# Performance work log

Measured on AMD Instinct MI355X. Metric: run time of the kernel, lower is better.

Reference implementation:

```python
import jax, jax.numpy as jnp
import numpy as np
from math import pi as PI

N = 50000      # nodes
E = 800000     # edges
G = 512        # graphs
L = 6          # num_layers
D = 128        # hidden_channels
F = 128        # num_filters
NG = 50        # num_gaussians
IN = 28        # input_dim
OUT = 32       # out_channels
CUT = 6.0      # cutoff
LN2 = float(np.log(2.0))
BN_EPS = 1e-5


def ssp(x):
    # ShiftedSoftplus
    return jax.nn.softplus(x) - LN2


def setup_inputs() -> dict:
    key = jax.random.key(0)
    ks = jax.random.split(key, 16)
    def rn(i, shape, s=0.05):
        return jax.random.normal(ks[i], shape, dtype=jnp.float32) * s
    return {
        "x": jax.random.normal(ks[0], (N, IN), dtype=jnp.float32),
        "pos": jax.random.normal(ks[1], (N, 3), dtype=jnp.float32) * 3.0,
        "batch": jnp.sort(jax.random.randint(ks[2], (N,), 0, G)),
        "edge_index": jax.random.randint(ks[3], (2, E), 0, N),
        # FeatureEmbedding: Linear(28,64) -> BN(64) -> ReLU -> Linear(64,128) -> ReLU
        "fe_w1": rn(4, (IN, D // 2)), "fe_b1": jnp.zeros((D // 2,), jnp.float32),
        "bn_gamma": jnp.ones((D // 2,), jnp.float32), "bn_beta": jnp.zeros((D // 2,), jnp.float32),
        "fe_w2": rn(5, (D // 2, D)), "fe_b2": jnp.zeros((D,), jnp.float32),
        # per-layer update_e: lin (no bias), mlp: Linear(NG,F)->SSP->Linear(F,F)
        "lin_w": rn(6, (L, D, F)),
        "mlp_w1": rn(7, (L, NG, F)), "mlp_b1": jnp.zeros((L, F), jnp.float32),
        "mlp_w2": rn(8, (L, F, F)), "mlp_b2": jnp.zeros((L, F), jnp.float32),
        # per-layer update_v: Linear(F,D)->SSP->Linear(D,D), residual
        "v1_w": rn(9, (L, F, D)), "v1_b": jnp.zeros((L, D), jnp.float32),
        "v2_w": rn(10, (L, D, D)), "v2_b": jnp.zeros((L, D), jnp.float32),
        # update_u: Linear(D,D//2)->SSP->Linear(D//2,OUT), then scatter over graphs
        "u1_w": rn(11, (D, D // 2)), "u1_b": jnp.zeros((D // 2,), jnp.float32),
        "u2_w": rn(12, (D // 2, OUT)), "u2_b": jnp.zeros((OUT,), jnp.float32),
    }


def reference(x, pos, batch, edge_index,
              fe_w1, fe_b1, bn_gamma, bn_beta, fe_w2, fe_b2,
              lin_w, mlp_w1, mlp_b1, mlp_w2, mlp_b2,
              v1_w, v1_b, v2_w, v2_b,
              u1_w, u1_b, u2_w, u2_b):
    row, col = edge_index[0], edge_index[1]  # (j, i): gather source j, scatter target i
    d = pos[row] - pos[col]                  # [E,3]
    dist = jnp.sqrt(jnp.sum(d * d, axis=-1))  # [E]
    offset = jnp.linspace(0.0, CUT, NG)
    coeff = -0.5 / (offset[1] - offset[0]) ** 2
    dist_emb = jnp.exp(coeff * (dist[:, None] - offset[None, :]) ** 2)  # [E,NG]
    cosC = 0.5 * (jnp.cos(dist * PI / CUT) + 1.0)                        # [E]

    # FeatureEmbedding (BatchNorm in training mode: batch statistics)
    h = x @ fe_w1 + fe_b1
    mu = jnp.mean(h, axis=0)
    var = jnp.mean((h - mu) ** 2, axis=0)
    h = (h - mu) / jnp.sqrt(var + BN_EPS) * bn_gamma + bn_beta
    h = jax.nn.relu(h)
    v = jax.nn.relu(h @ fe_w2 + fe_b2)  # [N,D]

    for l in range(L):
        # update_e: gate MLP on gaussian embedding, cosine cutoff, gather v[j]
        W = (ssp(dist_emb @ mlp_w1[l] + mlp_b1[l]) @ mlp_w2[l] + mlp_b2[l]) * cosC[:, None]  # [E,F]
        e = (v @ lin_w[l])[row] * W                                                          # [E,F]
        # update_v: scatter-add to nodes, MLP, residual
        agg = jax.ops.segment_sum(e, col, num_segments=N)                                    # [N,F]
        v = v + (ssp(agg @ v1_w[l] + v1_b[l]) @ v2_w[l] + v2_b[l])

    # update_u: per-node MLP then scatter-add per graph
    s = ssp(v @ u1_w + u1_b) @ u2_w + u2_b  # [N,OUT]
    return jax.ops.segment_sum(s, batch, num_segments=G)  # [G,OUT]
```

## Files before the change

### kernel.cpp

```cpp
#include <hip/hip_runtime.h>
#include <hip/hip_fp16.h>
#include <math.h>

#define DEV __device__ __forceinline__

constexpr int NGAUSS = 50;
constexpr int LAY = 6;
constexpr int K_TAB = 8192;
constexpr float DMAX = 40.0f;
constexpr float TSCALE = (float)(K_TAB - 1) / DMAX;
constexpr float STEP = 6.0f / 49.0f;
constexpr float COEFF = -0.5f / (STEP * STEP);
constexpr float LN2F = 0.69314718055994531f;
constexpr float PI_OVER_CUT = 0.52359877559829887f;

using f16x8 = __attribute__((ext_vector_type(8))) _Float16;
using f16x4 = __attribute__((ext_vector_type(4))) _Float16;
using f32x4 = __attribute__((ext_vector_type(4))) float;
using f32x8 = __attribute__((ext_vector_type(8))) float;

#define MFMA16(a, b, c) __builtin_amdgcn_mfma_f32_16x16x32_f16(a, b, c, 0, 0, 0)

DEV float sspf(float x) {
    float ax = fabsf(x);
    float e = __expf(-ax);
    return fmaxf(x, 0.f) + __logf(1.f + e) - LN2F;
}

DEV float4 ld_h4(const ushort* p) {
    uint2 r = *(const uint2*)p;
    __half2 a = __builtin_bit_cast(__half2, r.x);
    __half2 b = __builtin_bit_cast(__half2, r.y);
    float2 fa = __half22float2(a), fb = __half22float2(b);
    return make_float4(fa.x, fa.y, fb.x, fb.y);
}

__global__ void k_cvtT128(const float* __restrict__ src, ushort* __restrict__ dst) {
    const float* s = src + (size_t)blockIdx.x * 16384;
    ushort* d = dst + (size_t)blockIdx.x * 16384;
    for (int i = threadIdx.x; i < 16384; i += 256) {
        int k = i >> 7, c = i & 127;
        d[(c << 7) + k] = __builtin_bit_cast(ushort, (_Float16)s[i]);
    }
}
__global__ void k_cvtT_fe(const float* __restrict__ src, ushort* __restrict__ dst) {
    for (int i = threadIdx.x; i < 8192; i += 256) {
        int k = i >> 7, c = i & 127;
        dst[(c << 6) + k] = __builtin_bit_cast(ushort, (_Float16)src[i]);
    }
}
__global__ void k_cvtT_w1(const float* __restrict__ src, ushort* __restrict__ dst) {
    const float* s = src + (size_t)blockIdx.x * (NGAUSS * 128);
    ushort* d = dst + (size_t)blockIdx.x * (128 * 64);
    for (int i = threadIdx.x; i < 128 * 64; i += 256) {
        int c = i >> 6, k = i & 63;
        float v = (k < NGAUSS) ? s[k * 128 + c] : 0.f;
        d[(c << 6) + k] = __builtin_bit_cast(ushort, (_Float16)v);
    }
}

__global__ void k_hist(const int* __restrict__ ei, int* __restrict__ counts, int E) {
    int e = blockIdx.x * 256 + threadIdx.x;
    if (e < E) atomicAdd(&counts[ei[E + e]], 1);
}

__global__ void k_scan1(const int* __restrict__ counts, int* __restrict__ locex,
                        int* __restrict__ bsum, int n) {
    __shared__ int s_wsum[16];
    const int tid = threadIdx.x;
    const int i = blockIdx.x * 1024 + tid;
    const int lane = tid & 63, wv = tid >> 6;
    int v = (i < n) ? counts[i] : 0;
    int x = v;
    #pragma unroll
    for (int off = 1; off < 64; off <<= 1) {
        int y = __shfl_up(x, off, 64);
        if (lane >= off) x += y;
    }
    if (lane == 63) s_wsum[wv] = x;
    __syncthreads();
    if (wv == 0 && lane < 16) {
        int wval = s_wsum[lane];
        int wx = wval;
        #pragma unroll
        for (int off = 1; off < 16; off <<= 1) {
            int wy = __shfl_up(wx, off, 16);
            if (lane >= off) wx += wy;
        }
        s_wsum[lane] = wx - wval;
    }
    __syncthreads();
    if (i < n) locex[i] = s_wsum[wv] + x - v;
    if (tid == 1023) bsum[blockIdx.x] = s_wsum[15] + x;
}

__global__ void k_scan2(int* __restrict__ bsum, int nb) {
    __shared__ int s_wsum[16];
    const int tid = threadIdx.x;
    const int lane = tid & 63, wv = tid >> 6;
    int v = (tid < nb) ? bsum[tid] : 0;
    int x = v;
    #pragma unroll
    for (int off = 1; off < 64; off <<= 1) {
        int y = __shfl_up(x, off, 64);
        if (lane >= off) x += y;
    }
    if (lane == 63) s_wsum[wv] = x;
    __syncthreads();
    if (wv == 0 && lane < 16) {
        int wval = s_wsum[lane];
        int wx = wval;
        #pragma unroll
        for (int off = 1; off < 16; off <<= 1) {
            int wy = __shfl_up(wx, off, 16);
            if (lane >= off) wx += wy;
        }
        s_wsum[lane] = wx - wval;
    }
    __syncthreads();
    if (tid < nb) bsum[tid] = s_wsum[wv] + x - v;
}

__global__ void k_scan3(const int* __restrict__ locex, const int* __restrict__ bsumex,
                        int* __restrict__ cursor, int* __restrict__ rowptr, int n) {
    int i = blockIdx.x * 256 + threadIdx.x;
    if (i >= n) return;
    int e = locex[i] + bsumex[i >> 10];
    cursor[i] = e;
    rowptr[i] = e;
}

__global__ void k_scatter(const int* __restrict__ ei, const float* __restrict__ pos,
                          int* __restrict__ cursor, uint* __restrict__ s_ef, int E) {
    int e = blockIdx.x * 256 + threadIdx.x;
    if (e >= E) return;
    int r = ei[e], c = ei[E + e];
    int p = atomicAdd(&cursor[c], 1);
    float dx = pos[3 * r + 0] - pos[3 * c + 0];
    float dy = pos[3 * r + 1] - pos[3 * c + 1];
    float dz = pos[3 * r + 2] - pos[3 * c + 2];
    float d = sqrtf(dx * dx + dy * dy + dz * dz);
    int i0 = (int)(d * TSCALE + 0.5f);
    if (i0 > K_TAB - 1) i0 = K_TAB - 1;
    s_ef[p] = (uint)r | ((uint)i0 << 16);
}

__launch_bounds__(256)
__global__ void k_tab_all(const ushort* __restrict__ w1TA, const float* __restrict__ b1A,
                          const ushort* __restrict__ w2TA, const float* __restrict__ b2A,
                          ushort* __restrict__ tabA) {
    const int layer = blockIdx.x / (K_TAB / 32);
    const int k0 = (blockIdx.x % (K_TAB / 32)) * 32;
    const ushort* w1T = w1TA + (size_t)layer * 8192;
    const float* b1 = b1A + (size_t)layer * 128;
    const ushort* w2T = w2TA + (size_t)layer * 16384;
    const float* b2 = b2A + (size_t)layer * 128;
    ushort* tab = tabA + (size_t)layer * K_TAB * 128;

    constexpr int LDD = 72;
    constexpr int LDP = 136;
    __shared__ _Float16 sD[32 * LDD];
    __shared__ _Float16 sT[32 * LDP];
    __shared__ float s_cc[32];
    const int tid = threadIdx.x;

    for (int i = tid; i < 32 * 64; i += 256) {
        int r = i >> 6, g = i & 63;
        float val = 0.f;
        if (g < NGAUSS) {
            float d = (float)(k0 + r) * (1.0f / TSCALE);
            float t = d - g * STEP;
            val = __expf(COEFF * t * t);
        }
        sD[r * LDD + g] = (_Float16)val;
    }
    if (tid < 32) {
        float d = (float)(k0 + tid) * (1.0f / TSCALE);
        s_cc[tid] = 0.5f * (__cosf(d * PI_OVER_CUT) + 1.0f);
    }
    __syncthreads();

    const int wid = tid >> 6, lane = tid & 63;
    const int lr = lane & 15, lg = lane >> 4;
    const int kof = lg << 3;

    #pragma unroll
    for (int cb = 0; cb < 2; cb++) {
        const int col = ((2 * wid + cb) << 4) + lr;
        const ushort* bp = w1T + ((size_t)col << 6);
        f16x8 B0 = *(const f16x8*)(bp + kof);
        f16x8 B1 = *(const f16x8*)(bp + 32 + kof);
        float bb = b1[col];
        #pragma unroll
        for (int rt = 0; rt < 2; rt++) {
            const _Float16* ap = &sD[((rt << 4) + lr) * LDD + kof];
            f32x4 c = {0.f, 0.f, 0.f, 0.f};
            c = MFMA16(*(const f16x8*)ap, B0, c);
            c = MFMA16(*(const f16x8*)(ap + 32), B1, c);
            #pragma unroll
            for (int r = 0; r < 4; r++)
                sT[((rt << 4) + (lg << 2) + r) * LDP + col] = (_Float16)sspf(c[r] + bb);
        }
    }
    __syncthreads();

    #pragma unroll
    for (int cb = 0; cb < 2; cb++) {
        const int col = ((2 * wid + cb) << 4) + lr;
        const ushort* bp = w2T + ((size_t)col << 7);
        f16x8 B0 = *(const f16x8*)(bp + kof);
        f16x8 B1 = *(const f16x8*)(bp + 32 + kof);
        f16x8 B2 = *(const f16x8*)(bp + 64 + kof);
        f16x8 B3 = *(const f16x8*)(bp + 96 + kof);
        float bb = b2[col];
        #pragma unroll
        for (int rt = 0; rt < 2; rt++) {
            const _Float16* ap = &sT[((rt << 4) + lr) * LDP + kof];
            f32x4 c = {0.f, 0.f, 0.f, 0.f};
            c = MFMA16(*(const f16x8*)ap, B0, c);
            c = MFMA16(*(const f16x8*)(ap + 32), B1, c);
            c = MFMA16(*(const f16x8*)(ap + 64), B2, c);
            c = MFMA16(*(const f16x8*)(ap + 96), B3, c);
            #pragma unroll
            for (int r = 0; r < 4; r++) {
                int kr = (rt << 4) + (lg << 2) + r;
                tab[((size_t)(k0 + kr) << 7) + col] =
                    __builtin_bit_cast(ushort, (_Float16)((c[r] + bb) * s_cc[kr]));
            }
        }
    }
}

__launch_bounds__(256, 8)
__global__ void k_edge_csr(const uint* __restrict__ s_ef,
                           const int* __restrict__ rowptr, const int* __restrict__ counts,
                           const ushort* __restrict__ vlin, const ushort* __restrict__ tab,
                           ushort* __restrict__ agg, int N) {
    const int tid = threadIdx.x;
    const int l32 = tid & 31;
    const int h = l32 >> 4;
    const int lc = l32 & 15;
    const int n = blockIdx.x * 8 + (tid >> 5);
    if (n >= N) return;
    const ushort* tabc = tab + (lc << 3);
    const ushort* vlc  = vlin + (lc << 3);

    const int rs = rowptr[n];
    const int re = rs + counts[n];
    f32x8 acc = {0.f, 0.f, 0.f, 0.f, 0.f, 0.f, 0.f, 0.f};

    int e = rs + h;
    for (; e + 6 < re; e += 8) {
        f16x8 TP[4], VL[4];
        #pragma unroll
        for (int j = 0; j < 4; j++) {
            uint pk = s_ef[e + 2 * j];
            TP[j] = *(const f16x8*)(tabc + ((size_t)(pk >> 16) << 7));
            VL[j] = *(const f16x8*)(vlc + ((size_t)(pk & 0xFFFFu) << 7));
        }
        f16x8 p0 = TP[0] * VL[0];
        p0 += TP[1] * VL[1];
        f16x8 p1 = TP[2] * VL[2];
        p1 += TP[3] * VL[3];
        acc += __builtin_convertvector(p0, f32x8);
        acc += __builtin_convertvector(p1, f32x8);
    }
    for (; e < re; e += 2) {
        uint pk = s_ef[e];
        f16x8 tp = *(const f16x8*)(tabc + ((size_t)(pk >> 16) << 7));
        f16x8 vl = *(const f16x8*)(vlc + ((size_t)(pk & 0xFFFFu) << 7));
        acc += __builtin_convertvector(tp * vl, f32x8);
    }
    #pragma unroll
    for (int i = 0; i < 8; i++) acc[i] += __shfl_xor(acc[i], 16);
    if (h == 0) {
        f16x8 o;
        #pragma unroll
        for (int i = 0; i < 8; i++) o[i] = (_Float16)acc[i];
        *(f16x8*)&agg[((size_t)n << 7) + (lc << 3)] = o;
    }
}

__global__ void k_fe1(const float* __restrict__ x, const float* __restrict__ w,
                      const float* __restrict__ b, float* __restrict__ h, int N) {
    int idx = blockIdx.x * 256 + threadIdx.x;
    if (idx >= N * 64) return;
    int n = idx >> 6, c = idx & 63;
    const float* xr = x + (size_t)n * 28;
    float acc = b[c];
    #pragma unroll
    for (int k = 0; k < 28; k++) acc = fmaf(xr[k], w[k * 64 + c], acc);
    h[idx] = acc;
}

__global__ void k_bnstat(const float* __restrict__ h, float* __restrict__ stats, int N) {
    __shared__ float s_s[256], s_q[256];
    int tid = threadIdx.x;
    int c = tid & 63, g = tid >> 6;
    float s = 0.f, q = 0.f;
    for (int n = blockIdx.x * 4 + g; n < N; n += gridDim.x * 4) {
        float v = h[(size_t)n * 64 + c];
        s += v; q += v * v;
    }
    s_s[tid] = s; s_q[tid] = q;
    __syncthreads();
    if (tid < 64) {
        s = s_s[tid] + s_s[tid + 64] + s_s[tid + 128] + s_s[tid + 192];
        q = s_q[tid] + s_q[tid + 64] + s_q[tid + 128] + s_q[tid + 192];
        atomicAdd(&stats[tid], s);
        atomicAdd(&stats[64 + tid], q);
    }
}

__global__ void k_bnfin(const float* __restrict__ stats, float* __restrict__ prm,
                        const float* __restrict__ gamma, const float* __restrict__ beta,
                        float invN) {
    int c = threadIdx.x;
    float mu = stats[c] * invN;
    float var = stats[64 + c] * invN - mu * mu;
    float sc = gamma[c] * rsqrtf(var + 1e-5f);
    prm[c] = sc;
    prm[64 + c] = beta[c] - mu * sc;
}

__launch_bounds__(256, 4)
__global__ void k_fe2(const float* __restrict__ h, const float* __restrict__ prm,
                      const ushort* __restrict__ w2T, const float* __restrict__ b2,
                      ushort* __restrict__ v16, int N) {
    constexpr int LDP = 72;
    __shared__ _Float16 sH[64 * LDP];
    const int tid = threadIdx.x;
    const int n0 = blockIdx.x * 64;

    for (int i = tid; i < 64 * 16; i += 256) {
        int row = i >> 4, c4 = (i & 15) << 2;
        int gr = n0 + row;
        float4 hv = (gr < N) ? *(const float4*)&h[((size_t)gr << 6) + c4]
                             : make_float4(0.f, 0.f, 0.f, 0.f);
        float4 sc = *(const float4*)&prm[c4];
        float4 sh = *(const float4*)&prm[64 + c4];
        f16x4 o;
        o[0] = (_Float16)fmaxf(fmaf(hv.x, sc.x, sh.x), 0.f);
        o[1] = (_Float16)fmaxf(fmaf(hv.y, sc.y, sh.y), 0.f);
        o[2] = (_Float16)fmaxf(fmaf(hv.z, sc.z, sh.z), 0.f);
        o[3] = (_Float16)fmaxf(fmaf(hv.w, sc.w, sh.w), 0.f);
        *(f16x4*)&sH[row * LDP + c4] = o;
    }
    __syncthreads();

    const int wid = tid >> 6, lane = tid & 63;
    const int lr = lane & 15, lg = lane >> 4;
    const int kof = lg << 3;
    const int arow = wid * 16 + lr;
    const int drow0 = wid * 16 + (lg << 2);

    f16x8 a0 = *(const f16x8*)&sH[arow * LDP + kof];
    f16x8 a1 = *(const f16x8*)&sH[arow * LDP + 32 + kof];

    #pragma unroll
    for (int n = 0; n < 8; n++) {
        const ushort* bp = w2T + (((size_t)(n << 4) + lr) << 6);
        f32x4 c = {0.f, 0.f, 0.f, 0.f};
        c = MFMA16(a0, *(const f16x8*)(bp + kof), c);
        c = MFMA16(a1, *(const f16x8*)(bp + 32 + kof), c);
        int col = (n << 4) + lr;
        float bb = b2[col];
        #pragma unroll
        for (int r = 0; r < 4; r++) {
            int gr = n0 + drow0 + r;
            if (gr < N) v16[((size_t)gr << 7) + col] =
                __builtin_bit_cast(ushort, (_Float16)fmaxf(c[r] + bb, 0.f));
        }
    }
}

__launch_bounds__(256, 4)
__global__ void k_gemm_rb(const ushort* __restrict__ A, const ushort* __restrict__ wT,
                          ushort* __restrict__ C, int N) {
    constexpr int LDP = 136;
    __shared__ _Float16 sA[64 * LDP];
    const int tid = threadIdx.x;
    const int n0 = blockIdx.x * 64;

    for (int i = tid; i < 64 * 32; i += 256) {
        int row = i >> 5, c4 = (i & 31) << 2;
        int gr = n0 + row;
        uint2 val = (gr < N) ? *(const uint2*)&A[((size_t)gr << 7) + c4]
                             : make_uint2(0u, 0u);
        *(uint2*)&sA[row * LDP + c4] = val;
    }
    __syncthreads();

    const int wid = tid >> 6, lane = tid & 63;
    const int lr = lane & 15, lg = lane >> 4;
    const int kof = lg << 3;
    const int arow = wid * 16 + lr;
    const int drow0 = wid * 16 + (lg << 2);

    f16x8 a0 = *(const f16x8*)&sA[arow * LDP + kof];
    f16x8 a1 = *(const f16x8*)&sA[arow * LDP + 32 + kof];
    f16x8 a2 = *(const f16x8*)&sA[arow * LDP + 64 + kof];
    f16x8 a3 = *(const f16x8*)&sA[arow * LDP + 96 + kof];

    #pragma unroll
    for (int n = 0; n < 8; n++) {
        const ushort* bp = wT + (((size_t)(n << 4) + lr) << 7);
        f32x4 c = {0.f, 0.f, 0.f, 0.f};
        c = MFMA16(a0, *(const f16x8*)(bp + kof), c);
        c = MFMA16(a1, *(const f16x8*)(bp + 32 + kof), c);
        c = MFMA16(a2, *(const f16x8*)(bp + 64 + kof), c);
        c = MFMA16(a3, *(const f16x8*)(bp + 96 + kof), c);
        int col = (n << 4) + lr;
        #pragma unroll
        for (int r = 0; r < 4; r++) {
            int gr = n0 + drow0 + r;
            if (gr < N) C[((size_t)gr << 7) + col] =
                __builtin_bit_cast(ushort, (_Float16)c[r]);
        }
    }
}

__launch_bounds__(512, 8)
__global__ void k_update(const ushort* __restrict__ agg,
                         const ushort* __restrict__ w1T, const float* __restrict__ b1,
                         const ushort* __restrict__ w2T, const float* __restrict__ b2,
                         ushort* __restrict__ v16,
                         const ushort* __restrict__ linT, ushort* __restrict__ vlin, int N) {
    constexpr int LDP = 136;
    __shared__ _Float16 sA[64 * LDP];
    __shared__ _Float16 sB[64 * LDP];
    const int tid = threadIdx.x;
    const int n0 = blockIdx.x * 64;

    for (int i = tid; i < 64 * 32; i += 512) {
        int row = i >> 5, c4 = (i & 31) << 2;
        int gr = n0 + row;
        uint2 a = (gr < N) ? *(const uint2*)&agg[((size_t)gr << 7) + c4] : make_uint2(0u, 0u);
        uint2 b = (gr < N) ? *(const uint2*)&v16[((size_t)gr << 7) + c4] : make_uint2(0u, 0u);
        *(uint2*)&sA[row * LDP + c4] = a;
        *(uint2*)&sB[row * LDP + c4] = b;
    }
    __syncthreads();

    const int wid = tid >> 6, lane = tid & 63;
    const int lr = lane & 15, lg = lane >> 4;
    const int kof = lg << 3;
    const int col = (wid << 4) + lr;
    const int dr0 = lg << 2;

    f32x4 acc[4];

    {
        const ushort* bp = w1T + ((size_t)col << 7);
        f16x8 B0 = *(const f16x8*)(bp + kof);
        f16x8 B1 = *(const f16x8*)(bp + 32 + kof);
        f16x8 B2 = *(const f16x8*)(bp + 64 + kof);
        f16x8 B3 = *(const f16x8*)(bp + 96 + kof);
        #pragma unroll
        for (int rb = 0; rb < 4; rb++) {
            const _Float16* ap = &sA[((rb << 4) + lr) * LDP + kof];
            f32x4 c = {0.f, 0.f, 0.f, 0.f};
            c = MFMA16(*(const f16x8*)ap, B0, c);
            c = MFMA16(*(const f16x8*)(ap + 32), B1, c);
            c = MFMA16(*(const f16x8*)(ap + 64), B2, c);
            c = MFMA16(*(const f16x8*)(ap + 96), B3, c);
            acc[rb] = c;
        }
    }
    __syncthreads();
    {
        float bb = b1[col];
        #pragma unroll
        for (int rb = 0; rb < 4; rb++) {
            #pragma unroll
            for (int r = 0; r < 4; r++)
                sA[((rb << 4) + dr0 + r) * LDP + col] = (_Float16)sspf(acc[rb][r] + bb);
        }
    }
    __syncthreads();

    {
        const ushort* bp = w2T + ((size_t)col << 7);
        f16x8 B0 = *(const f16x8*)(bp + kof);
        f16x8 B1 = *(const f16x8*)(bp + 32 + kof);
        f16x8 B2 = *(const f16x8*)(bp + 64 + kof);
        f16x8 B3 = *(const f16x8*)(bp + 96 + kof);
        #pragma unroll
        for (int rb = 0; rb < 4; rb++) {
            const _Float16* ap = &sA[((rb << 4) + lr) * LDP + kof];
            f32x4 c = {0.f, 0.f, 0.f, 0.f};
            c = MFMA16(*(const f16x8*)ap, B0, c);
            c = MFMA16(*(const f16x8*)(ap + 32), B1, c);
            c = MFMA16(*(const f16x8*)(ap + 64), B2, c);
            c = MFMA16(*(const f16x8*)(ap + 96), B3, c);
            acc[rb] = c;
        }
    }
    {
        float bb = b2[col];
        #pragma unroll
        for (int rb = 0; rb < 4; rb++) {
            #pragma unroll
            for (int r = 0; r < 4; r++) {
                _Float16* p = &sB[((rb << 4) + dr0 + r) * LDP + col];
                *p = (_Float16)(acc[rb][r] + bb + (float)*p);
            }
        }
    }
    __syncthreads();

    for (int i = tid; i < 64 * 32; i += 512) {
        int row = i >> 5, c4 = (i & 31) << 2;
        int gr = n0 + row;
        if (gr < N) *(uint2*)&v16[((size_t)gr << 7) + c4] = *(const uint2*)&sB[row * LDP + c4];
    }
    if (!linT) return;

    {
        const ushort* bp = linT + ((size_t)col << 7);
        f16x8 B0 = *(const f16x8*)(bp + kof);
        f16x8 B1 = *(const f16x8*)(bp + 32 + kof);
        f16x8 B2 = *(const f16x8*)(bp + 64 + kof);
        f16x8 B3 = *(const f16x8*)(bp + 96 + kof);
        #pragma unroll
        for (int rb = 0; rb < 4; rb++) {
            const _Float16* ap = &sB[((rb << 4) + lr) * LDP + kof];
            f32x4 c = {0.f, 0.f, 0.f, 0.f};
            c = MFMA16(*(const f16x8*)ap, B0, c);
            c = MFMA16(*(const f16x8*)(ap + 32), B1, c);
            c = MFMA16(*(const f16x8*)(ap + 64), B2, c);
            c = MFMA16(*(const f16x8*)(ap + 96), B3, c);
            acc[rb] = c;
        }
    }
    #pragma unroll
    for (int rb = 0; rb < 4; rb++) {
        #pragma unroll
        for (int r = 0; r < 4; r++)
            sA[((rb << 4) + dr0 + r) * LDP + col] = (_Float16)acc[rb][r];
    }
    __syncthreads();

    for (int i = tid; i < 64 * 32; i += 512) {
        int row = i >> 5, c4 = (i & 31) << 2;
        int gr = n0 + row;
        if (gr < N) *(uint2*)&vlin[((size_t)gr << 7) + c4] = *(const uint2*)&sA[row * LDP + c4];
    }
}

__launch_bounds__(256, 4)
__global__ void k_uout(const ushort* __restrict__ v16, const float* __restrict__ u1w,
                       const float* __restrict__ u1b, const float* __restrict__ u2w,
                       const float* __restrict__ u2b, const int* __restrict__ batch,
                       float* __restrict__ out, int N) {
    __shared__ float sA[64 * 128];
    const int tid = threadIdx.x;
    const int n0 = blockIdx.x * 64;

    for (int i = tid; i < 64 * 32; i += 256) {
        int row = i >> 5, cq = (i & 31) << 2;
        int gr = n0 + row;
        float4 val = make_float4(0.f, 0.f, 0.f, 0.f);
        if (gr < N) val = ld_h4(&v16[((size_t)gr << 7) + cq]);
        *(float4*)&sA[row * 128 + cq] = val;
    }
    __syncthreads();

    const int cg = tid & 31, rg = tid >> 5;
    const int r0 = rg << 3;
    const int c2 = cg << 1;

    float2 acc[8];
    {
        float2 b1v = *(const float2*)&u1b[c2];
        #pragma unroll
        for (int i = 0; i < 8; i++) acc[i] = b1v;
        #pragma unroll 4
        for (int k = 0; k < 128; k++) {
            float2 wv = *(const float2*)&u1w[(k << 6) + c2];
            #pragma unroll
            for (int i = 0; i < 8; i++) {
                float a = sA[(r0 + i) * 128 + k];
                acc[i].x = fmaf(a, wv.x, acc[i].x);
                acc[i].y = fmaf(a, wv.y, acc[i].y);
            }
        }
    }
    __syncthreads();
    #pragma unroll
    for (int i = 0; i < 8; i++) {
        sA[(r0 + i) * 64 + c2 + 0] = sspf(acc[i].x);
        sA[(r0 + i) * 64 + c2 + 1] = sspf(acc[i].y);
    }
    __syncthreads();

    float acc2[8];
    {
        float bb = u2b[cg];
        #pragma unroll
        for (int i = 0; i < 8; i++) acc2[i] = bb;
        #pragma unroll 4
        for (int k = 0; k < 64; k++) {
            float wv = u2w[(k << 5) + cg];
            #pragma unroll
            for (int i = 0; i < 8; i++)
                acc2[i] = fmaf(sA[(r0 + i) * 64 + k], wv, acc2[i]);
        }
    }

    int cur = -1;
    float run = 0.f;
    #pragma unroll
    for (int i = 0; i < 8; i++) {
        int gr = n0 + r0 + i;
        int g = (gr < N) ? batch[gr] : -1;
        if (g != cur) {
            if (cur >= 0) atomicAdd(&out[(size_t)cur * 32 + cg], run);
            cur = g;
            run = 0.f;
        }
        if (g >= 0) run += acc2[i];
    }
    if (cur >= 0) atomicAdd(&out[(size_t)cur * 32 + cg], run);
}

extern "C" void kernel_launch(void* const* d_in, const int* in_sizes, int n_in,
                              void* d_out, int out_size, void* d_ws, size_t ws_size,
                              hipStream_t stream) {
    const float* x      = (const float*)d_in[0];
    const float* pos    = (const float*)d_in[1];
    const int*   batch  = (const int*)d_in[2];
    const int*   ei     = (const int*)d_in[3];
    const float* fe_w1  = (const float*)d_in[4];
    const float* fe_b1  = (const float*)d_in[5];
    const float* bn_g   = (const float*)d_in[6];
    const float* bn_b   = (const float*)d_in[7];
    const float* fe_w2  = (const float*)d_in[8];
    const float* fe_b2  = (const float*)d_in[9];
    const float* lin_w  = (const float*)d_in[10];
    const float* mlp_w1 = (const float*)d_in[11];
    const float* mlp_b1 = (const float*)d_in[12];
    const float* mlp_w2 = (const float*)d_in[13];
    const float* mlp_b2 = (const float*)d_in[14];
    const float* v1_w   = (const float*)d_in[15];
    const float* v1_b   = (const float*)d_in[16];
    const float* v2_w   = (const float*)d_in[17];
    const float* v2_b   = (const float*)d_in[18];
    const float* u1_w   = (const float*)d_in[19];
    const float* u1_b   = (const float*)d_in[20];
    const float* u2_w   = (const float*)d_in[21];
    const float* u2_b   = (const float*)d_in[22];

    const int N = in_sizes[0] / 28;
    const int E = in_sizes[3] / 2;
    const int NB1 = (N + 1023) / 1024;

    char* ws = (char*)d_ws;
    size_t o = 0;
    auto alloc = [&](size_t bytes) { void* p = ws + o; o += (bytes + 255) & ~(size_t)255; return p; };
    int*    counts = (int*)   alloc((size_t)N * 4);
    int*    cursor = (int*)   alloc((size_t)N * 4);
    int*    rowptr = (int*)   alloc((size_t)N * 4);
    int*    bsum   = (int*)   alloc((size_t)NB1 * 4);
    uint*   s_ef   = (uint*)  alloc((size_t)E * 4);
    float*  stats  = (float*) alloc(128 * 4);
    float*  prm    = (float*) alloc(128 * 4);
    ushort* tab    = (ushort*)alloc((size_t)LAY * K_TAB * 128 * 2);
    ushort* v16    = (ushort*)alloc((size_t)N * 128 * 2);
    ushort* vlin   = (ushort*)alloc((size_t)N * 128 * 2);
    ushort* agg    = (ushort*)alloc((size_t)N * 128 * 2);
    float*  h      = (float*) alloc((size_t)N * 64 * 4);
    int*    locex  = (int*)   alloc((size_t)N * 4);
    ushort* v1T    = (ushort*)alloc((size_t)LAY * 16384 * 2);
    ushort* v2T    = (ushort*)alloc((size_t)LAY * 16384 * 2);
    ushort* linT   = (ushort*)alloc((size_t)LAY * 16384 * 2);
    ushort* mw2T   = (ushort*)alloc((size_t)LAY * 16384 * 2);
    ushort* mw1T   = (ushort*)alloc((size_t)LAY * 8192 * 2);
    ushort* fe2T   = (ushort*)alloc((size_t)8192 * 2);

    k_cvtT128<<<LAY, 256, 0, stream>>>(v1_w, v1T);
    k_cvtT128<<<LAY, 256, 0, stream>>>(v2_w, v2T);
    k_cvtT128<<<LAY, 256, 0, stream>>>(lin_w, linT);
    k_cvtT128<<<LAY, 256, 0, stream>>>(mlp_w2, mw2T);
    k_cvtT_w1<<<LAY, 256, 0, stream>>>(mlp_w1, mw1T);
    k_cvtT_fe<<<1, 256, 0, stream>>>(fe_w2, fe2T);

    hipMemsetAsync(counts, 0, (size_t)N * 4, stream);
    k_hist<<<(E + 255) / 256, 256, 0, stream>>>(ei, counts, E);
    k_scan1<<<NB1, 1024, 0, stream>>>(counts, locex, bsum, N);
    k_scan2<<<1, 1024, 0, stream>>>(bsum, NB1);
    k_scan3<<<(N + 255) / 256, 256, 0, stream>>>(locex, bsum, cursor, rowptr, N);
    k_scatter<<<(E + 255) / 256, 256, 0, stream>>>(ei, pos, cursor, s_ef, E);

    k_tab_all<<<LAY * (K_TAB / 32), 256, 0, stream>>>(mw1T, mlp_b1, mw2T, mlp_b2, tab);

    hipMemsetAsync(stats, 0, 128 * 4, stream);
    k_fe1<<<(N * 64 + 255) / 256, 256, 0, stream>>>(x, fe_w1, fe_b1, h, N);
    k_bnstat<<<256, 256, 0, stream>>>(h, stats, N);
    k_bnfin<<<1, 64, 0, stream>>>(stats, prm, bn_g, bn_b, 1.0f / (float)N);
    const int gblk = (N + 63) / 64;
    k_fe2<<<gblk, 256, 0, stream>>>(h, prm, fe2T, fe_b2, v16, N);

    k_gemm_rb<<<gblk, 256, 0, stream>>>(v16, linT, vlin, N);

    const int eblk = (N + 7) / 8;
    for (int l = 0; l < LAY; l++) {
        k_edge_csr<<<eblk, 256, 0, stream>>>(
            s_ef, rowptr, counts, vlin,
            tab + (size_t)l * K_TAB * 128, agg, N);
        const ushort* lin_next = (l + 1 < LAY) ? linT + (size_t)(l + 1) * 16384 : nullptr;
        k_update<<<gblk, 512, 0, stream>>>(
            agg, v1T + (size_t)l * 16384, v1_b + (size_t)l * 128,
            v2T + (size_t)l * 16384, v2_b + (size_t)l * 128,
            v16, lin_next, vlin, N);
    }

    hipMemsetAsync(d_out, 0, (size_t)out_size * 4, stream);
    k_uout<<<gblk, 256, 0, stream>>>(v16, u1_w, u1_b, u2_w, u2_b, batch, (float*)d_out, N);
}
```

Before: 601.4 us.

## Record atomic rank in histogram and widen edge aggregation to one wavefront per node

The histogram kernel now stores each edge's atomic rank, so the scatter computes its CSR slot as rowptr plus rank and no longer needs a second atomic pass or a cursor array. The per-node edge aggregation kernel now assigns a full 64-lane wavefront (four edge streams) to each node instead of half a wavefront (two streams), with an extra cross-lane shuffle reduction. This aims to cut contended atomics in setup and raise memory-level parallelism in the gather loop. The cost is an extra E-sized rank buffer and more idle lanes on nodes with few edges.

```diff
diff --git a/kernel.cpp b/kernel.cpp
--- a/kernel.cpp
+++ b/kernel.cpp
@@ -59,9 +59,10 @@
     }
 }
 
-__global__ void k_hist(const int* __restrict__ ei, int* __restrict__ counts, int E) {
+__global__ void k_hist(const int* __restrict__ ei, int* __restrict__ counts,
+                       int* __restrict__ rank, int E) {
     int e = blockIdx.x * 256 + threadIdx.x;
-    if (e < E) atomicAdd(&counts[ei[E + e]], 1);
+    if (e < E) rank[e] = atomicAdd(&counts[ei[E + e]], 1);
 }
 
 __global__ void k_scan1(const int* __restrict__ counts, int* __restrict__ locex,
@@ -122,26 +123,25 @@
 }
 
 __global__ void k_scan3(const int* __restrict__ locex, const int* __restrict__ bsumex,
-                        int* __restrict__ cursor, int* __restrict__ rowptr, int n) {
+                        int* __restrict__ rowptr, int n) {
     int i = blockIdx.x * 256 + threadIdx.x;
     if (i >= n) return;
-    int e = locex[i] + bsumex[i >> 10];
-    cursor[i] = e;
-    rowptr[i] = e;
+    rowptr[i] = locex[i] + bsumex[i >> 10];
 }
 
 __global__ void k_scatter(const int* __restrict__ ei, const float* __restrict__ pos,
-                          int* __restrict__ cursor, uint* __restrict__ s_ef, int E) {
+                          const int* __restrict__ rowptr, const int* __restrict__ rank,
+                          uint* __restrict__ s_ef, int E) {
     int e = blockIdx.x * 256 + threadIdx.x;
     if (e >= E) return;
     int r = ei[e], c = ei[E + e];
-    int p = atomicAdd(&cursor[c], 1);
     float dx = pos[3 * r + 0] - pos[3 * c + 0];
     float dy = pos[3 * r + 1] - pos[3 * c + 1];
     float dz = pos[3 * r + 2] - pos[3 * c + 2];
     float d = sqrtf(dx * dx + dy * dy + dz * dz);
     int i0 = (int)(d * TSCALE + 0.5f);
     if (i0 > K_TAB - 1) i0 = K_TAB - 1;
+    int p = rowptr[c] + rank[e];
     s_ef[p] = (uint)r | ((uint)i0 << 16);
 }
 
@@ -237,10 +237,10 @@
                            const ushort* __restrict__ vlin, const ushort* __restrict__ tab,
                            ushort* __restrict__ agg, int N) {
     const int tid = threadIdx.x;
-    const int l32 = tid & 31;
-    const int h = l32 >> 4;
-    const int lc = l32 & 15;
-    const int n = blockIdx.x * 8 + (tid >> 5);
+    const int lane = tid & 63;
+    const int h = lane >> 4;
+    const int lc = lane & 15;
+    const int n = blockIdx.x * 4 + (tid >> 6);
     if (n >= N) return;
     const ushort* tabc = tab + (lc << 3);
     const ushort* vlc  = vlin + (lc << 3);
@@ -250,11 +250,11 @@
     f32x8 acc = {0.f, 0.f, 0.f, 0.f, 0.f, 0.f, 0.f, 0.f};
 
     int e = rs + h;
-    for (; e + 6 < re; e += 8) {
+    for (; e + 12 < re; e += 16) {
         f16x8 TP[4], VL[4];
         #pragma unroll
         for (int j = 0; j < 4; j++) {
-            uint pk = s_ef[e + 2 * j];
+            uint pk = s_ef[e + 4 * j];
             TP[j] = *(const f16x8*)(tabc + ((size_t)(pk >> 16) << 7));
             VL[j] = *(const f16x8*)(vlc + ((size_t)(pk & 0xFFFFu) << 7));
         }
@@ -265,14 +265,17 @@
         acc += __builtin_convertvector(p0, f32x8);
         acc += __builtin_convertvector(p1, f32x8);
     }
-    for (; e < re; e += 2) {
+    for (; e < re; e += 4) {
         uint pk = s_ef[e];
         f16x8 tp = *(const f16x8*)(tabc + ((size_t)(pk >> 16) << 7));
         f16x8 vl = *(const f16x8*)(vlc + ((size_t)(pk & 0xFFFFu) << 7));
         acc += __builtin_convertvector(tp * vl, f32x8);
     }
     #pragma unroll
-    for (int i = 0; i < 8; i++) acc[i] += __shfl_xor(acc[i], 16);
+    for (int i = 0; i < 8; i++) {
+        acc[i] += __shfl_xor(acc[i], 16);
+        acc[i] += __shfl_xor(acc[i], 32);
+    }
     if (h == 0) {
         f16x8 o;
         #pragma unroll
@@ -659,9 +662,9 @@
     size_t o = 0;
     auto alloc = [&](size_t bytes) { void* p = ws + o; o += (bytes + 255) & ~(size_t)255; return p; };
     int*    counts = (int*)   alloc((size_t)N * 4);
-    int*    cursor = (int*)   alloc((size_t)N * 4);
     int*    rowptr = (int*)   alloc((size_t)N * 4);
     int*    bsum   = (int*)   alloc((size_t)NB1 * 4);
+    int*    rank   = (int*)   alloc((size_t)E * 4);
     uint*   s_ef   = (uint*)  alloc((size_t)E * 4);
     float*  stats  = (float*) alloc(128 * 4);
     float*  prm    = (float*) alloc(128 * 4);
@@ -686,11 +689,11 @@
     k_cvtT_fe<<<1, 256, 0, stream>>>(fe_w2, fe2T);
 
     hipMemsetAsync(counts, 0, (size_t)N * 4, stream);
-    k_hist<<<(E + 255) / 256, 256, 0, stream>>>(ei, counts, E);
+    k_hist<<<(E + 255) / 256, 256, 0, stream>>>(ei, counts, rank, E);
     k_scan1<<<NB1, 1024, 0, stream>>>(counts, locex, bsum, N);
     k_scan2<<<1, 1024, 0, stream>>>(bsum, NB1);
-    k_scan3<<<(N + 255) / 256, 256, 0, stream>>>(locex, bsum, cursor, rowptr, N);
-    k_scatter<<<(E + 255) / 256, 256, 0, stream>>>(ei, pos, cursor, s_ef, E);
+    k_scan3<<<(N + 255) / 256, 256, 0, stream>>>(locex, bsum, rowptr, N);
+    k_scatter<<<(E + 255) / 256, 256, 0, stream>>>(ei, pos, rowptr, rank, s_ef, E);
 
     k_tab_all<<<LAY * (K_TAB / 32), 256, 0, stream>>>(mw1T, mlp_b1, mw2T, mlp_b2, tab);
 
@@ -703,7 +706,7 @@
 
     k_gemm_rb<<<gblk, 256, 0, stream>>>(v16, linT, vlin, N);
 
-    const int eblk = (N + 7) / 8;
+    const int eblk = (N + 3) / 4;
     for (int l = 0; l < LAY; l++) {
         k_edge_csr<<<eblk, 256, 0, stream>>>(
             s_ef, rowptr, counts, vlin,
```

Measured after the change: 590.4 us. About the same (-1.8%).
